# Performance work log

Measured on AMD Instinct MI355X. Metric: run time of the kernel, lower is better.

The kernel has to match this reference:

```python
import jax, jax.numpy as jnp
import numpy as np

N_NODES = 50000
N_EDGES = 1000000
D = 66
NEG_SLOPE = 0.2
EPS_BN = 1e-5


def _glorot(key, shape):
    fan = sum(shape)
    lim = jnp.sqrt(6.0 / fan)
    return jax.random.uniform(key, shape, jnp.float32, -lim, lim)


def setup_inputs() -> dict:
    key = jax.random.key(0)
    ks = jax.random.split(key, 40)
    inp = {
        'h': jax.random.normal(ks[0], (N_NODES, D), jnp.float32),
        'edge_index': jax.random.randint(ks[1], (2, N_EDGES), 0, N_NODES, jnp.int32),
        'edge_weight': jax.random.uniform(ks[2], (N_EDGES, 1), jnp.float32),
        'bn_gamma': jnp.ones((D,), jnp.float32),
        'bn_beta': jnp.zeros((D,), jnp.float32),
    }
    i = 3
    for l in (1, 2, 3):
        inp[f'W{l}'] = _glorot(ks[i], (D, D)); i += 1
        inp[f'b{l}'] = jnp.zeros((D,), jnp.float32)
        inp[f'att_src{l}'] = _glorot(ks[i], (D,)); i += 1
        inp[f'att_dst{l}'] = _glorot(ks[i], (D,)); i += 1
        inp[f'We{l}'] = _glorot(ks[i], (1, D)); i += 1
        inp[f'att_e{l}'] = _glorot(ks[i], (D,)); i += 1
    dims = [(D, D), (D, D), (D, D), (D, D), (D, 22)]
    for l, (din, dout) in enumerate(dims, start=1):
        inp[f'fc{l}_w'] = _glorot(ks[i], (din, dout)); i += 1
        inp[f'fc{l}_b'] = jnp.zeros((dout,), jnp.float32)
    return inp


def _gat_conv(h, src, dst, edge_weight, W, b, att_src, att_dst, We, att_e):
    x = h @ W                                     # [N, D]
    a_src = x @ att_src                           # [N]
    a_dst = x @ att_dst                           # [N]
    a_e = (edge_weight @ We) @ att_e              # [E]
    alpha = a_src[src] + a_dst[dst] + a_e         # [E]
    alpha = jnp.where(alpha > 0, alpha, NEG_SLOPE * alpha)
    # scatter-softmax over destination nodes
    m = jax.ops.segment_max(alpha, dst, num_segments=N_NODES)
    m = jnp.where(jnp.isfinite(m), m, 0.0)
    ex = jnp.exp(alpha - m[dst])
    denom = jax.ops.segment_sum(ex, dst, num_segments=N_NODES)
    coef = ex / (denom[dst] + 1e-16)              # [E]
    out = jax.ops.segment_sum(coef[:, None] * x[src], dst, num_segments=N_NODES)
    return out + b


def reference(h, edge_index, edge_weight, bn_gamma, bn_beta,
              W1, b1, att_src1, att_dst1, We1, att_e1,
              W2, b2, att_src2, att_dst2, We2, att_e2,
              W3, b3, att_src3, att_dst3, We3, att_e3,
              fc1_w, fc1_b, fc2_w, fc2_b, fc3_w, fc3_b,
              fc4_w, fc4_b, fc5_w, fc5_b):
    src, dst = edge_index[0], edge_index[1]
    # BatchNorm1d (training-mode batch statistics, biased variance)
    mean = h.mean(0)
    var = ((h - mean) ** 2).mean(0)
    x = (h - mean) * jax.lax.rsqrt(var + EPS_BN) * bn_gamma + bn_beta
    x = jax.nn.relu(_gat_conv(x, src, dst, edge_weight, W1, b1, att_src1, att_dst1, We1, att_e1))
    x = jax.nn.relu(_gat_conv(x, src, dst, edge_weight, W2, b2, att_src2, att_dst2, We2, att_e2))
    x = jax.nn.relu(_gat_conv(x, src, dst, edge_weight, W3, b3, att_src3, att_dst3, We3, att_e3))
    x = jax.nn.relu(x @ fc1_w + fc1_b)
    x = jax.nn.relu(x @ fc2_w + fc2_b)
    x = jax.nn.relu(x @ fc3_w + fc3_b)
    x = jax.nn.relu(x @ fc4_w + fc4_b)
    return x @ fc5_w + fc5_b
```

## Files before the change

kernel.cpp:

```cpp
#include <hip/hip_runtime.h>
#include <math.h>

#define D 66
#define SP 68
#define NEG_SLOPE 0.2f
#define CAP 6144

typedef short s8v __attribute__((ext_vector_type(8)));
typedef float f4v __attribute__((ext_vector_type(4)));

__device__ __forceinline__ float lrelu(float a){ return a > 0.f ? a : NEG_SLOPE * a; }
__device__ __forceinline__ void fma4(float4& a, float s, const float4& w){
  a.x = fmaf(s, w.x, a.x); a.y = fmaf(s, w.y, a.y);
  a.z = fmaf(s, w.z, a.z); a.w = fmaf(s, w.w, a.w);
}
__device__ __forceinline__ unsigned short bf16r(float f){
  unsigned u = __float_as_uint(f);
  u += 0x7FFFu + ((u >> 16) & 1u);
  return (unsigned short)(u >> 16);
}
__device__ __forceinline__ float bf16f(unsigned short b){
  return __uint_as_float(((unsigned)b) << 16);
}
__device__ __forceinline__ void split8(const float* p, s8v& a0, s8v& a1, s8v& a2){
  #pragma unroll
  for (int j = 0; j < 8; j++){
    float v = p[j];
    unsigned short b0 = bf16r(v);  float f0 = bf16f(b0);
    float r1 = v - f0;
    unsigned short b1 = bf16r(r1); float f1 = bf16f(b1);
    unsigned short b2 = bf16r(r1 - f1);
    a0[j] = (short)b0; a1[j] = (short)b1; a2[j] = (short)b2;
  }
}
#define MM6(acc, a0, a1, a2, b0v, b1v, b2v)                                \
  acc = __builtin_amdgcn_mfma_f32_16x16x32_bf16(a0, b0v, acc, 0, 0, 0);    \
  acc = __builtin_amdgcn_mfma_f32_16x16x32_bf16(a1, b0v, acc, 0, 0, 0);    \
  acc = __builtin_amdgcn_mfma_f32_16x16x32_bf16(a0, b1v, acc, 0, 0, 0);    \
  acc = __builtin_amdgcn_mfma_f32_16x16x32_bf16(a2, b0v, acc, 0, 0, 0);    \
  acc = __builtin_amdgcn_mfma_f32_16x16x32_bf16(a1, b1v, acc, 0, 0, 0);    \
  acc = __builtin_amdgcn_mfma_f32_16x16x32_bf16(a0, b2v, acc, 0, 0, 0);

__global__ __launch_bounds__(256) void k_bn_stats(const float* __restrict__ h,
                                                  float* __restrict__ sums, int n){
  __shared__ float ls[2 * D];
  int t = threadIdx.x;
  if (t < 2 * D) ls[t] = 0.f;
  __syncthreads();
  int rpb = (n + gridDim.x - 1) / gridDim.x;
  int r0 = blockIdx.x * rpb;
  int r1 = min(n, r0 + rpb);
  if (t < 3 * D){
    int c = t % D, seg = t / D;
    float s1 = 0.f, s2 = 0.f;
    for (int r = r0 + seg; r < r1; r += 3){
      float v = h[(size_t)r * D + c];
      s1 += v; s2 += v * v;
    }
    atomicAdd(&ls[c], s1);
    atomicAdd(&ls[D + c], s2);
  }
  __syncthreads();
  if (t < 2 * D) atomicAdd(&sums[t], ls[t]);
}

__global__ void k_bn_finalize(const float* __restrict__ sums,
                              const float* __restrict__ gamma, const float* __restrict__ beta,
                              const float* __restrict__ We1, const float* __restrict__ ae1,
                              const float* __restrict__ We2, const float* __restrict__ ae2,
                              const float* __restrict__ We3, const float* __restrict__ ae3,
                              float* __restrict__ misc, int n){
  int t = threadIdx.x;
  if (t < D){
    float mean = sums[t] / (float)n;
    float var  = sums[D + t] / (float)n - mean * mean;
    float inv  = rsqrtf(var + 1e-5f);
    float sc = gamma[t] * inv;
    misc[t] = sc;
    misc[D + t] = beta[t] - mean * sc;
  } else if (t == D){
    float c = 0.f; for (int d = 0; d < D; d++) c += We1[d] * ae1[d]; misc[2*D + 0] = c;
  } else if (t == D + 1){
    float c = 0.f; for (int d = 0; d < D; d++) c += We2[d] * ae2[d]; misc[2*D + 1] = c;
  } else if (t == D + 2){
    float c = 0.f; for (int d = 0; d < D; d++) c += We3[d] * ae3[d]; misc[2*D + 2] = c;
  }
}

__global__ __launch_bounds__(256) void k_bn_apply(const float* __restrict__ h, const float* __restrict__ misc,
                                                  float* __restrict__ x, int n){
  int i = blockIdx.x * 256 + threadIdx.x;
  int r = i / (SP/2), c2 = i - r * (SP/2);
  if (r >= n) return;
  int c = 2 * c2;
  float2 v = make_float2(0.f, 0.f);
  if (c < D){
    float2 hv = *(const float2*)&h[(size_t)r * D + c];
    v.x = hv.x * misc[c]     + misc[D + c];
    v.y = hv.y * misc[c + 1] + misc[D + c + 1];
  }
  *(float2*)&x[(size_t)r * SP + c] = v;
}

__global__ __launch_bounds__(256) void k_pack(const float* __restrict__ w0, const float* __restrict__ w1,
                                              const float* __restrict__ w2,
                                              short* __restrict__ W0, short* __restrict__ W1,
                                              short* __restrict__ W2){
  int tid = blockIdx.x * 256 + threadIdx.x;
  if (tid >= 3 * 15 * 64) return;
  int L = tid & 63;
  int ct = (tid >> 6) % 15;
  int lay = tid / 960;
  const float* w = (lay == 0) ? w0 : ((lay == 1) ? w1 : w2);
  int c = ct / 5, t = ct % 5;
  int nn = t * 16 + (L & 15);
  int kb = c * 32 + (L >> 4) * 8;
  #pragma unroll
  for (int j = 0; j < 8; j++){
    int k = kb + j;
    float v = (k < D && nn < D) ? w[k * D + nn] : 0.f;
    unsigned short b0 = bf16r(v);  float f0 = bf16f(b0);
    float r1 = v - f0;
    unsigned short b1 = bf16r(r1); float f1 = bf16f(b1);
    unsigned short b2 = bf16r(r1 - f1);
    W0[tid * 8 + j] = (short)b0;
    W1[tid * 8 + j] = (short)b1;
    W2[tid * 8 + j] = (short)b2;
  }
}

__global__ __launch_bounds__(256) void k_packfc(const float* __restrict__ w0, const float* __restrict__ w1,
                                                const float* __restrict__ w2, const float* __restrict__ w3,
                                                const float* __restrict__ w4,
                                                short* __restrict__ W0, short* __restrict__ W1,
                                                short* __restrict__ W2){
  int tid = blockIdx.x * 256 + threadIdx.x;
  if (tid >= 5 * 15 * 64) return;
  int L = tid & 63;
  int ct = (tid >> 6) % 15;
  int lay = tid / 960;
  const float* w = (lay == 0) ? w0 : (lay == 1) ? w1 : (lay == 2) ? w2 : (lay == 3) ? w3 : w4;
  int ncol = (lay == 4) ? 22 : D;
  int c = ct / 5, t = ct % 5;
  int nn = t * 16 + (L & 15);
  int kb = c * 32 + (L >> 4) * 8;
  #pragma unroll
  for (int j = 0; j < 8; j++){
    int k = kb + j;
    float v = (k < D && nn < ncol) ? w[k * ncol + nn] : 0.f;
    unsigned short b0 = bf16r(v);  float f0 = bf16f(b0);
    float r1 = v - f0;
    unsigned short b1 = bf16r(r1); float f1 = bf16f(b1);
    unsigned short b2 = bf16r(r1 - f1);
    W0[tid * 8 + j] = (short)b0;
    W1[tid * 8 + j] = (short)b1;
    W2[tid * 8 + j] = (short)b2;
  }
}

__global__ __launch_bounds__(256) void k_hist(const int* __restrict__ dst,
                                              int* __restrict__ bhist, int E){
  __shared__ int h[256];
  int t = threadIdx.x;
  h[t] = 0;
  __syncthreads();
  int stride = gridDim.x * blockDim.x;
  for (int e = blockIdx.x * blockDim.x + t; e < E; e += stride)
    atomicAdd(&h[dst[e] >> 8], 1);
  __syncthreads();
  if (h[t]) atomicAdd(&bhist[t], h[t]);
}

__global__ void k_bscan(const int* __restrict__ bhist, int* __restrict__ bbase,
                        int* __restrict__ gcur, int* __restrict__ rowptr, int N, int E){
  __shared__ int sh[256];
  int t = threadIdx.x;
  int v = bhist[t];
  sh[t] = v; __syncthreads();
  for (int o = 1; o < 256; o <<= 1){
    int u = (t >= o) ? sh[t - o] : 0;
    __syncthreads();
    sh[t] += u;
    __syncthreads();
  }
  int ex = sh[t] - v;
  bbase[t] = ex;
  gcur[t] = ex;
  if (t == 255){ bbase[256] = sh[255]; rowptr[N] = E; }
}

#define PCHUNK 4096
__global__ __launch_bounds__(256) void k_part(const int* __restrict__ src, const int* __restrict__ dst,
                                              const float* __restrict__ ew,
                                              int* __restrict__ gcur, int2* __restrict__ tmp, int E){
  __shared__ int hist[256];
  __shared__ int base[256];
  int t = threadIdx.x;
  int e0 = blockIdx.x * PCHUNK;
  int eend = min(E, e0 + PCHUNK);
  hist[t] = 0;
  __syncthreads();
  for (int e = e0 + t; e < eend; e += 256)
    atomicAdd(&hist[dst[e] >> 8], 1);
  __syncthreads();
  if (hist[t] > 0) base[t] = atomicAdd(&gcur[t], hist[t]);
  hist[t] = 0;
  __syncthreads();
  for (int e = e0 + t; e < eend; e += 256){
    int d = dst[e];
    int b = d >> 8;
    int off = atomicAdd(&hist[b], 1);
    tmp[base[b] + off] = make_int2((src[e] & 0xffff) | ((d & 255) << 16), __float_as_int(ew[e]));
  }
}

__global__ __launch_bounds__(256) void k_bsort(const int2* __restrict__ tmp, const int* __restrict__ bbase,
                                               int2* __restrict__ epair, int* __restrict__ rowptr, int N){
  __shared__ int2 ebuf[CAP];
  __shared__ int lcnt[256];
  __shared__ int sc[256];
  __shared__ int lcur[256];
  int b = blockIdx.x, t = threadIdx.x;
  int s0 = bbase[b], s1 = bbase[b + 1];
  int cnt = s1 - s0;
  lcnt[t] = 0;
  __syncthreads();
  for (int j = t; j < cnt; j += 256){
    int2 e = tmp[s0 + j];
    if (j < CAP) ebuf[j] = e;
    atomicAdd(&lcnt[(e.x >> 16) & 255], 1);
  }
  __syncthreads();
  int v = lcnt[t];
  sc[t] = v; __syncthreads();
  for (int o = 1; o < 256; o <<= 1){
    int u = (t >= o) ? sc[t - o] : 0;
    __syncthreads();
    sc[t] += u;
    __syncthreads();
  }
  int ex = sc[t] - v;
  int node = (b << 8) + t;
  if (node < N) rowptr[node] = s0 + ex;
  lcur[t] = ex;
  __syncthreads();
  for (int j = t; j < cnt; j += 256){
    int2 e = (j < CAP) ? ebuf[j] : tmp[s0 + j];
    int i = (e.x >> 16) & 255;
    int p = atomicAdd(&lcur[i], 1);
    epair[s0 + p] = make_int2(e.x & 0xffff, e.y);
  }
}

__global__ __launch_bounds__(256) void k_mm(const float* __restrict__ X,
    const short* __restrict__ W0, const short* __restrict__ W1, const short* __restrict__ W2,
    const float* __restrict__ att_s, const float* __restrict__ att_d,
    float* __restrict__ Y, float* __restrict__ a_src, float* __restrict__ a_dst, int n){
  const int wv = threadIdx.x >> 6, L = threadIdx.x & 63;
  const int quad = L >> 4, m = L & 15;
  const int row0 = blockIdx.x * 64 + wv * 16;
  const int lrow = min(row0 + m, n - 1);
  const float* xr = X + (size_t)lrow * SP;
  f4v acc[5];
  #pragma unroll
  for (int t = 0; t < 5; t++) acc[t] = (f4v){0.f,0.f,0.f,0.f};

  #pragma unroll
  for (int c = 0; c < 3; c++){
    float xv[8];
    if (c < 2){
      float4 p0 = *(const float4*)&xr[c * 32 + quad * 8];
      float4 p1 = *(const float4*)&xr[c * 32 + quad * 8 + 4];
      xv[0] = p0.x; xv[1] = p0.y; xv[2] = p0.z; xv[3] = p0.w;
      xv[4] = p1.x; xv[5] = p1.y; xv[6] = p1.z; xv[7] = p1.w;
    } else {
      float4 p0 = make_float4(0.f, 0.f, 0.f, 0.f);
      if (quad == 0) p0 = *(const float4*)&xr[64];
      xv[0] = p0.x; xv[1] = p0.y; xv[2] = p0.z; xv[3] = p0.w;
      xv[4] = 0.f; xv[5] = 0.f; xv[6] = 0.f; xv[7] = 0.f;
    }
    s8v a0, a1, a2;
    split8(xv, a0, a1, a2);
    const short* b0p = W0 + (c * 5) * 512 + L * 8;
    const short* b1p = W1 + (c * 5) * 512 + L * 8;
    const short* b2p = W2 + (c * 5) * 512 + L * 8;
    #pragma unroll
    for (int t = 0; t < 5; t++){
      s8v b0v = *(const s8v*)(b0p + t * 512);
      s8v b1v = *(const s8v*)(b1p + t * 512);
      s8v b2v = *(const s8v*)(b2p + t * 512);
      MM6(acc[t], a0, a1, a2, b0v, b1v, b2v)
    }
  }

  float ps[4] = {0.f,0.f,0.f,0.f}, pd[4] = {0.f,0.f,0.f,0.f};
  #pragma unroll
  for (int t = 0; t < 5; t++){
    int col = t * 16 + m;
    float as_v = 0.f, ad_v = 0.f;
    if (col < D){ as_v = att_s[col]; ad_v = att_d[col]; }
    #pragma unroll
    for (int r = 0; r < 4; r++){
      ps[r] += acc[t][r] * as_v;
      pd[r] += acc[t][r] * ad_v;
    }
  }
  #pragma unroll
  for (int r = 0; r < 4; r++){
    int rw = row0 + quad * 4 + r;
    if (rw < n){
      float* yr = Y + (size_t)rw * SP;
      #pragma unroll
      for (int t = 0; t < 4; t++) yr[t * 16 + m] = acc[t][r];
      if (m < 4) yr[64 + m] = (m < 2) ? acc[4][r] : 0.f;
    }
  }
  #pragma unroll
  for (int o = 1; o <= 8; o <<= 1){
    #pragma unroll
    for (int r = 0; r < 4; r++){
      ps[r] += __shfl_xor(ps[r], o);
      pd[r] += __shfl_xor(pd[r], o);
    }
  }
  if (m == 0){
    #pragma unroll
    for (int r = 0; r < 4; r++){
      int rw = row0 + quad * 4 + r;
      if (rw < n){ a_src[rw] = ps[r]; a_dst[rw] = pd[r]; }
    }
  }
}

template<bool LAST>
__global__ __launch_bounds__(256) void k_fcl(const float* __restrict__ X,
    const short* __restrict__ W0, const short* __restrict__ W1, const short* __restrict__ W2,
    const float* __restrict__ bias,
    float* __restrict__ Y, int n){
  const int wv = threadIdx.x >> 6, L = threadIdx.x & 63;
  const int quad = L >> 4, m = L & 15;
  const int row0 = blockIdx.x * 64 + wv * 16;
  const int lrow = min(row0 + m, n - 1);
  const float* xr = X + (size_t)lrow * SP;
  constexpr int NT = LAST ? 2 : 5;
  f4v acc[NT];
  #pragma unroll
  for (int t = 0; t < NT; t++) acc[t] = (f4v){0.f,0.f,0.f,0.f};

  #pragma unroll
  for (int c = 0; c < 3; c++){
    float xv[8];
    if (c < 2){
      float4 p0 = *(const float4*)&xr[c * 32 + quad * 8];
      float4 p1 = *(const float4*)&xr[c * 32 + quad * 8 + 4];
      xv[0] = p0.x; xv[1] = p0.y; xv[2] = p0.z; xv[3] = p0.w;
      xv[4] = p1.x; xv[5] = p1.y; xv[6] = p1.z; xv[7] = p1.w;
    } else {
      float4 p0 = make_float4(0.f, 0.f, 0.f, 0.f);
      if (quad == 0) p0 = *(const float4*)&xr[64];
      xv[0] = p0.x; xv[1] = p0.y; xv[2] = p0.z; xv[3] = p0.w;
      xv[4] = 0.f; xv[5] = 0.f; xv[6] = 0.f; xv[7] = 0.f;
    }
    s8v a0, a1, a2;
    split8(xv, a0, a1, a2);
    const short* b0p = W0 + (c * 5) * 512 + L * 8;
    const short* b1p = W1 + (c * 5) * 512 + L * 8;
    const short* b2p = W2 + (c * 5) * 512 + L * 8;
    #pragma unroll
    for (int t = 0; t < NT; t++){
      s8v b0v = *(const s8v*)(b0p + t * 512);
      s8v b1v = *(const s8v*)(b1p + t * 512);
      s8v b2v = *(const s8v*)(b2p + t * 512);
      MM6(acc[t], a0, a1, a2, b0v, b1v, b2v)
    }
  }

  if (!LAST){
    #pragma unroll
    for (int r = 0; r < 4; r++){
      int rw = row0 + quad * 4 + r;
      if (rw < n){
        float* yr = Y + (size_t)rw * SP;
        #pragma unroll
        for (int t = 0; t < 4; t++){
          int col = t * 16 + m;
          float v = acc[t][r] + bias[col];
          yr[col] = v > 0.f ? v : 0.f;
        }
        if (m < 4){
          float v = 0.f;
          if (m < 2){
            v = acc[4][r] + bias[64 + m];
            v = v > 0.f ? v : 0.f;
          }
          yr[64 + m] = v;
        }
      }
    }
  } else {
    #pragma unroll
    for (int t = 0; t < 2; t++){
      int col = t * 16 + m;
      #pragma unroll
      for (int r = 0; r < 4; r++){
        int rw = row0 + quad * 4 + r;
        if (col < 22 && rw < n) Y[(size_t)rw * 22 + col] = acc[t][r] + bias[col];
      }
    }
  }
}

__global__ __launch_bounds__(256) void k_agg(const float* __restrict__ y,
                                             const float* __restrict__ a_src, const float* __restrict__ a_dst,
                                             const int* __restrict__ rowptr, const int2* __restrict__ epair,
                                             const float* __restrict__ misc, int cidx,
                                             const float* __restrict__ bias,
                                             float* __restrict__ xout, int n){
  const int wid  = (int)((blockIdx.x * (size_t)blockDim.x + threadIdx.x) >> 6);
  const int lane = threadIdx.x & 63;
  if (wid >= n) return;
  const int beg = rowptr[wid];
  const int deg = rowptr[wid + 1] - beg;
  const float ce  = misc[2 * D + cidx];
  const float adn = a_dst[wid];
  const int g = lane >> 4, q = lane & 15;

  float4 vacc = make_float4(0.f, 0.f, 0.f, 0.f);
  float2 tacc = make_float2(0.f, 0.f);

  if (deg <= 64){
    int s = 0; float al = -INFINITY;
    bool act = lane < deg;
    if (act){
      int2 ep = epair[beg + lane];
      s = ep.x;
      al = lrelu(a_src[s] + adn + ce * __int_as_float(ep.y));
    }
    float m = al;
    #pragma unroll
    for (int o = 32; o; o >>= 1) m = fmaxf(m, __shfl_xor(m, o));
    float ex = act ? __expf(al - m) : 0.f;
    float sum = ex;
    #pragma unroll
    for (int o = 32; o; o >>= 1) sum += __shfl_xor(sum, o);
    float coef = ex * (1.f / (sum + 1e-16f));
    for (int e0 = 0; e0 < deg; e0 += 4){
      int e = e0 + g;
      int   st = __shfl(s, e);
      float ct = __shfl(coef, e);
      const float* row = y + (size_t)st * SP;
      float4 yv = *(const float4*)&row[4 * q];
      fma4(vacc, ct, yv);
      if (q == 0){
        float2 tv = *(const float2*)&row[64];
        tacc.x += ct * tv.x; tacc.y += ct * tv.y;
      }
    }
  } else {
    float m = -INFINITY;
    for (int j0 = 0; j0 < deg; j0 += 64){
      int j = j0 + lane;
      if (j < deg){
        int2 ep = epair[beg + j];
        m = fmaxf(m, lrelu(a_src[ep.x] + adn + ce * __int_as_float(ep.y)));
      }
    }
    #pragma unroll
    for (int o = 32; o; o >>= 1) m = fmaxf(m, __shfl_xor(m, o));
    float sum = 0.f;
    for (int j0 = 0; j0 < deg; j0 += 64){
      int j = j0 + lane;
      if (j < deg){
        int2 ep = epair[beg + j];
        sum += __expf(lrelu(a_src[ep.x] + adn + ce * __int_as_float(ep.y)) - m);
      }
    }
    #pragma unroll
    for (int o = 32; o; o >>= 1) sum += __shfl_xor(sum, o);
    float inv = 1.f / (sum + 1e-16f);
    for (int j0 = 0; j0 < deg; j0 += 64){
      int cnt = min(64, deg - j0);
      int s = 0; float coef = 0.f;
      if (lane < cnt){
        int2 ep = epair[beg + j0 + lane];
        s = ep.x;
        coef = __expf(lrelu(a_src[s] + adn + ce * __int_as_float(ep.y)) - m) * inv;
      }
      for (int e0 = 0; e0 < cnt; e0 += 4){
        int e = e0 + g;
        int   st = __shfl(s, e);
        float ct = __shfl(coef, e);
        const float* row = y + (size_t)st * SP;
        float4 yv = *(const float4*)&row[4 * q];
        fma4(vacc, ct, yv);
        if (q == 0){
          float2 tv = *(const float2*)&row[64];
          tacc.x += ct * tv.x; tacc.y += ct * tv.y;
        }
      }
    }
  }

  #pragma unroll
  for (int o = 16; o <= 32; o <<= 1){
    vacc.x += __shfl_xor(vacc.x, o);
    vacc.y += __shfl_xor(vacc.y, o);
    vacc.z += __shfl_xor(vacc.z, o);
    vacc.w += __shfl_xor(vacc.w, o);
    tacc.x += __shfl_xor(tacc.x, o);
    tacc.y += __shfl_xor(tacc.y, o);
  }
  float* orow = xout + (size_t)wid * SP;
  if (lane < 16){
    float4 v;
    v.x = vacc.x + bias[4*lane+0]; v.x = v.x > 0.f ? v.x : 0.f;
    v.y = vacc.y + bias[4*lane+1]; v.y = v.y > 0.f ? v.y : 0.f;
    v.z = vacc.z + bias[4*lane+2]; v.z = v.z > 0.f ? v.z : 0.f;
    v.w = vacc.w + bias[4*lane+3]; v.w = v.w > 0.f ? v.w : 0.f;
    *(float4*)&orow[4 * lane] = v;
  }
  if (lane == 0){
    float4 tv;
    tv.x = tacc.x + bias[64]; tv.x = tv.x > 0.f ? tv.x : 0.f;
    tv.y = tacc.y + bias[65]; tv.y = tv.y > 0.f ? tv.y : 0.f;
    tv.z = 0.f; tv.w = 0.f;
    *(float4*)&orow[64] = tv;
  }
}

extern "C" void kernel_launch(void* const* d_in, const int* in_sizes, int n_in,
                              void* d_out, int out_size, void* d_ws, size_t ws_size,
                              hipStream_t stream){
  const float* h     = (const float*)d_in[0];
  const int*   ei    = (const int*)  d_in[1];
  const float* ew    = (const float*)d_in[2];
  const float* gamma = (const float*)d_in[3];
  const float* beta  = (const float*)d_in[4];
  const float *Wl[3], *bl[3], *asl[3], *adl[3], *Wel[3], *ael[3];
  int idx = 5;
  for (int l = 0; l < 3; l++){
    Wl[l]  = (const float*)d_in[idx++];
    bl[l]  = (const float*)d_in[idx++];
    asl[l] = (const float*)d_in[idx++];
    adl[l] = (const float*)d_in[idx++];
    Wel[l] = (const float*)d_in[idx++];
    ael[l] = (const float*)d_in[idx++];
  }
  const float *fw[5], *fb[5];
  for (int l = 0; l < 5; l++){ fw[l] = (const float*)d_in[idx++]; fb[l] = (const float*)d_in[idx++]; }

  int N = in_sizes[0] / D;
  int E = in_sizes[1] / 2;
  const int* src  = ei;
  const int* dstp = ei + E;

  char* base = (char*)d_ws;
  size_t o = 0;
  auto alloc = [&](size_t b){ size_t r = o; o += (b + 255) & ~(size_t)255; return r; };
  float*  bufA   = (float*)(base + alloc((size_t)N * SP * 4));
  float*  bufB   = (float*)(base + alloc((size_t)N * SP * 4));
  float*  a_src  = (float*)(base + alloc((size_t)N * 4));
  float*  a_dst  = (float*)(base + alloc((size_t)N * 4));
  float*  misc   = (float*)(base + alloc(512 * 4));
  float*  sums   = (float*)(base + alloc(2 * D * 4));
  int*    rowptr = (int*)  (base + alloc((size_t)(N + 1) * 4));
  int*    bhist  = (int*)  (base + alloc(256 * 4));
  int*    bbase  = (int*)  (base + alloc(257 * 4));
  int*    gcur   = (int*)  (base + alloc(256 * 4));
  int2*   epair  = (int2*) (base + alloc((size_t)E * 8));
  short*  W0p    = (short*)(base + alloc(3 * 7680 * 2));
  short*  W1p    = (short*)(base + alloc(3 * 7680 * 2));
  short*  W2p    = (short*)(base + alloc(3 * 7680 * 2));
  short*  FW0p   = (short*)(base + alloc(5 * 7680 * 2));
  short*  FW1p   = (short*)(base + alloc(5 * 7680 * 2));
  short*  FW2p   = (short*)(base + alloc(5 * 7680 * 2));
  int2*   tmp    = (int2*)bufB;

  hipMemsetAsync(sums, 0, 2 * D * 4, stream);
  hipMemsetAsync(bhist, 0, 256 * 4, stream);

  k_bn_stats<<<256, 256, 0, stream>>>(h, sums, N);
  k_bn_finalize<<<1, 128, 0, stream>>>(sums, gamma, beta, Wel[0], ael[0], Wel[1], ael[1], Wel[2], ael[2], misc, N);
  k_pack<<<12, 256, 0, stream>>>(Wl[0], Wl[1], Wl[2], W0p, W1p, W2p);
  k_packfc<<<19, 256, 0, stream>>>(fw[0], fw[1], fw[2], fw[3], fw[4], FW0p, FW1p, FW2p);

  int NB = (N + 255) >> 8;
  k_hist<<<256, 256, 0, stream>>>(dstp, bhist, E);
  k_bscan<<<1, 256, 0, stream>>>(bhist, bbase, gcur, rowptr, N, E);
  k_part<<<(E + PCHUNK - 1) / PCHUNK, 256, 0, stream>>>(src, dstp, ew, gcur, tmp, E);
  k_bsort<<<NB, 256, 0, stream>>>(tmp, bbase, epair, rowptr, N);

  int bnb = ((size_t)N * (SP/2) + 255) / 256;
  k_bn_apply<<<bnb, 256, 0, stream>>>(h, misc, bufA, N);

  int gb = (N + 63) / 64;
  int ab = (N + 3) / 4;

  for (int l = 0; l < 3; l++){
    k_mm<<<gb, 256, 0, stream>>>(bufA, W0p + l * 7680, W1p + l * 7680, W2p + l * 7680,
                                 asl[l], adl[l], bufB, a_src, a_dst, N);
    k_agg<<<ab, 256, 0, stream>>>(bufB, a_src, a_dst, rowptr, epair, misc, l, bl[l], bufA, N);
  }

  k_fcl<false><<<gb, 256, 0, stream>>>(bufA, FW0p + 0 * 7680, FW1p + 0 * 7680, FW2p + 0 * 7680, fb[0], bufB, N);
  k_fcl<false><<<gb, 256, 0, stream>>>(bufB, FW0p + 1 * 7680, FW1p + 1 * 7680, FW2p + 1 * 7680, fb[1], bufA, N);
  k_fcl<false><<<gb, 256, 0, stream>>>(bufA, FW0p + 2 * 7680, FW1p + 2 * 7680, FW2p + 2 * 7680, fb[2], bufB, N);
  k_fcl<false><<<gb, 256, 0, stream>>>(bufB, FW0p + 3 * 7680, FW1p + 3 * 7680, FW2p + 3 * 7680, fb[3], bufA, N);
  k_fcl<true ><<<gb, 256, 0, stream>>>(bufA, FW0p + 4 * 7680, FW1p + 4 * 7680, FW2p + 4 * 7680, fb[4], (float*)d_out, N);
}
```

Measured before the change: 490.3 us.

## Fuse five FC layers into one kernel and widen aggregation edge groups

The five separate fully-connected layer launches are replaced by one kernel that keeps each 64-row tile's intermediate activations in shared memory across layers. This removes four launches and the global-memory round trips of the intermediates. The FC biases are packed into a padded buffer by the weight-pack kernel. Separately, the GAT aggregation now processes 8 edges per step with 8 lanes per row, each lane loading two float4s, instead of 4 edges with 16 lanes. This aims to give more gathers in flight per wave, at the cost of more register use and an extra shuffle-reduction stage.

```diff
diff --git a/kernel.cpp b/kernel.cpp
--- a/kernel.cpp
+++ b/kernel.cpp
@@ -132,29 +132,39 @@
 __global__ __launch_bounds__(256) void k_packfc(const float* __restrict__ w0, const float* __restrict__ w1,
                                                 const float* __restrict__ w2, const float* __restrict__ w3,
                                                 const float* __restrict__ w4,
+                                                const float* __restrict__ b0, const float* __restrict__ b1,
+                                                const float* __restrict__ b2, const float* __restrict__ b3,
+                                                const float* __restrict__ b4,
                                                 short* __restrict__ W0, short* __restrict__ W1,
-                                                short* __restrict__ W2){
+                                                short* __restrict__ W2, float* __restrict__ bpack){
   int tid = blockIdx.x * 256 + threadIdx.x;
-  if (tid >= 5 * 15 * 64) return;
-  int L = tid & 63;
-  int ct = (tid >> 6) % 15;
-  int lay = tid / 960;
-  const float* w = (lay == 0) ? w0 : (lay == 1) ? w1 : (lay == 2) ? w2 : (lay == 3) ? w3 : w4;
-  int ncol = (lay == 4) ? 22 : D;
-  int c = ct / 5, t = ct % 5;
-  int nn = t * 16 + (L & 15);
-  int kb = c * 32 + (L >> 4) * 8;
-  #pragma unroll
-  for (int j = 0; j < 8; j++){
-    int k = kb + j;
-    float v = (k < D && nn < ncol) ? w[k * ncol + nn] : 0.f;
-    unsigned short b0 = bf16r(v);  float f0 = bf16f(b0);
-    float r1 = v - f0;
-    unsigned short b1 = bf16r(r1); float f1 = bf16f(b1);
-    unsigned short b2 = bf16r(r1 - f1);
-    W0[tid * 8 + j] = (short)b0;
-    W1[tid * 8 + j] = (short)b1;
-    W2[tid * 8 + j] = (short)b2;
+  if (tid < 5 * 15 * 64){
+    int L = tid & 63;
+    int ct = (tid >> 6) % 15;
+    int lay = tid / 960;
+    const float* w = (lay == 0) ? w0 : (lay == 1) ? w1 : (lay == 2) ? w2 : (lay == 3) ? w3 : w4;
+    int ncol = (lay == 4) ? 22 : D;
+    int c = ct / 5, t = ct % 5;
+    int nn = t * 16 + (L & 15);
+    int kb = c * 32 + (L >> 4) * 8;
+    #pragma unroll
+    for (int j = 0; j < 8; j++){
+      int k = kb + j;
+      float v = (k < D && nn < ncol) ? w[k * ncol + nn] : 0.f;
+      unsigned short bb0 = bf16r(v);  float f0 = bf16f(bb0);
+      float r1 = v - f0;
+      unsigned short bb1 = bf16r(r1); float f1 = bf16f(bb1);
+      unsigned short bb2 = bf16r(r1 - f1);
+      W0[tid * 8 + j] = (short)bb0;
+      W1[tid * 8 + j] = (short)bb1;
+      W2[tid * 8 + j] = (short)bb2;
+    }
+  } else if (tid < 5 * 15 * 64 + 400){
+    int i = tid - 5 * 15 * 64;
+    int lay = i / 80, col = i % 80;
+    const float* b = (lay == 0) ? b0 : (lay == 1) ? b1 : (lay == 2) ? b2 : (lay == 3) ? b3 : b4;
+    int ncol = (lay == 4) ? 22 : D;
+    bpack[i] = (col < ncol) ? b[col] : 0.f;
   }
 }
 
@@ -332,79 +342,82 @@
   }
 }
 
-template<bool LAST>
-__global__ __launch_bounds__(256) void k_fcl(const float* __restrict__ X,
+#define FST 84
+__global__ __launch_bounds__(256) void k_fcmm(const float* __restrict__ X,
     const short* __restrict__ W0, const short* __restrict__ W1, const short* __restrict__ W2,
-    const float* __restrict__ bias,
-    float* __restrict__ Y, int n){
+    const float* __restrict__ bpack, float* __restrict__ out, int n){
+  __shared__ __align__(16) float xs[4][16][FST];
   const int wv = threadIdx.x >> 6, L = threadIdx.x & 63;
   const int quad = L >> 4, m = L & 15;
   const int row0 = blockIdx.x * 64 + wv * 16;
   const int lrow = min(row0 + m, n - 1);
   const float* xr = X + (size_t)lrow * SP;
-  constexpr int NT = LAST ? 2 : 5;
-  f4v acc[NT];
-  #pragma unroll
-  for (int t = 0; t < NT; t++) acc[t] = (f4v){0.f,0.f,0.f,0.f};
-
-  #pragma unroll
-  for (int c = 0; c < 3; c++){
-    float xv[8];
-    if (c < 2){
-      float4 p0 = *(const float4*)&xr[c * 32 + quad * 8];
-      float4 p1 = *(const float4*)&xr[c * 32 + quad * 8 + 4];
-      xv[0] = p0.x; xv[1] = p0.y; xv[2] = p0.z; xv[3] = p0.w;
-      xv[4] = p1.x; xv[5] = p1.y; xv[6] = p1.z; xv[7] = p1.w;
+
+  for (int l = 0; l < 5; l++){
+    const int NTl = (l == 4) ? 2 : 5;
+    f4v acc[5];
+    #pragma unroll
+    for (int t = 0; t < 5; t++) acc[t] = (f4v){0.f,0.f,0.f,0.f};
+    #pragma unroll
+    for (int c = 0; c < 3; c++){
+      float xv[8];
+      if (l == 0){
+        if (c < 2){
+          float4 p0 = *(const float4*)&xr[c * 32 + quad * 8];
+          float4 p1 = *(const float4*)&xr[c * 32 + quad * 8 + 4];
+          xv[0] = p0.x; xv[1] = p0.y; xv[2] = p0.z; xv[3] = p0.w;
+          xv[4] = p1.x; xv[5] = p1.y; xv[6] = p1.z; xv[7] = p1.w;
+        } else {
+          float4 p0 = make_float4(0.f, 0.f, 0.f, 0.f);
+          if (quad == 0) p0 = *(const float4*)&xr[64];
+          xv[0] = p0.x; xv[1] = p0.y; xv[2] = p0.z; xv[3] = p0.w;
+          xv[4] = 0.f; xv[5] = 0.f; xv[6] = 0.f; xv[7] = 0.f;
+        }
+      } else {
+        if (c == 2 && quad >= 2){
+          #pragma unroll
+          for (int j = 0; j < 8; j++) xv[j] = 0.f;
+        } else {
+          float4 p0 = *(const float4*)&xs[wv][m][c * 32 + quad * 8];
+          float4 p1 = *(const float4*)&xs[wv][m][c * 32 + quad * 8 + 4];
+          xv[0] = p0.x; xv[1] = p0.y; xv[2] = p0.z; xv[3] = p0.w;
+          xv[4] = p1.x; xv[5] = p1.y; xv[6] = p1.z; xv[7] = p1.w;
+        }
+      }
+      s8v a0, a1, a2;
+      split8(xv, a0, a1, a2);
+      const short* b0p = W0 + ((l * 3 + c) * 5) * 512 + L * 8;
+      const short* b1p = W1 + ((l * 3 + c) * 5) * 512 + L * 8;
+      const short* b2p = W2 + ((l * 3 + c) * 5) * 512 + L * 8;
+      for (int t = 0; t < NTl; t++){
+        s8v b0v = *(const s8v*)(b0p + t * 512);
+        s8v b1v = *(const s8v*)(b1p + t * 512);
+        s8v b2v = *(const s8v*)(b2p + t * 512);
+        MM6(acc[t], a0, a1, a2, b0v, b1v, b2v)
+      }
+    }
+    if (l < 4){
+      __syncthreads();
+      #pragma unroll
+      for (int t = 0; t < 5; t++){
+        int col = t * 16 + m;
+        float bv = bpack[l * 80 + col];
+        #pragma unroll
+        for (int r = 0; r < 4; r++){
+          float v = acc[t][r] + bv;
+          xs[wv][quad * 4 + r][col] = v > 0.f ? v : 0.f;
+        }
+      }
+      __syncthreads();
     } else {
-      float4 p0 = make_float4(0.f, 0.f, 0.f, 0.f);
-      if (quad == 0) p0 = *(const float4*)&xr[64];
-      xv[0] = p0.x; xv[1] = p0.y; xv[2] = p0.z; xv[3] = p0.w;
-      xv[4] = 0.f; xv[5] = 0.f; xv[6] = 0.f; xv[7] = 0.f;
-    }
-    s8v a0, a1, a2;
-    split8(xv, a0, a1, a2);
-    const short* b0p = W0 + (c * 5) * 512 + L * 8;
-    const short* b1p = W1 + (c * 5) * 512 + L * 8;
-    const short* b2p = W2 + (c * 5) * 512 + L * 8;
-    #pragma unroll
-    for (int t = 0; t < NT; t++){
-      s8v b0v = *(const s8v*)(b0p + t * 512);
-      s8v b1v = *(const s8v*)(b1p + t * 512);
-      s8v b2v = *(const s8v*)(b2p + t * 512);
-      MM6(acc[t], a0, a1, a2, b0v, b1v, b2v)
-    }
-  }
-
-  if (!LAST){
-    #pragma unroll
-    for (int r = 0; r < 4; r++){
-      int rw = row0 + quad * 4 + r;
-      if (rw < n){
-        float* yr = Y + (size_t)rw * SP;
+      #pragma unroll
+      for (int t = 0; t < 2; t++){
+        int col = t * 16 + m;
         #pragma unroll
-        for (int t = 0; t < 4; t++){
-          int col = t * 16 + m;
-          float v = acc[t][r] + bias[col];
-          yr[col] = v > 0.f ? v : 0.f;
+        for (int r = 0; r < 4; r++){
+          int rw = row0 + quad * 4 + r;
+          if (col < 22 && rw < n) out[(size_t)rw * 22 + col] = acc[t][r] + bpack[4 * 80 + col];
         }
-        if (m < 4){
-          float v = 0.f;
-          if (m < 2){
-            v = acc[4][r] + bias[64 + m];
-            v = v > 0.f ? v : 0.f;
-          }
-          yr[64 + m] = v;
-        }
-      }
-    }
-  } else {
-    #pragma unroll
-    for (int t = 0; t < 2; t++){
-      int col = t * 16 + m;
-      #pragma unroll
-      for (int r = 0; r < 4; r++){
-        int rw = row0 + quad * 4 + r;
-        if (col < 22 && rw < n) Y[(size_t)rw * 22 + col] = acc[t][r] + bias[col];
       }
     }
   }
@@ -423,10 +436,11 @@
   const int deg = rowptr[wid + 1] - beg;
   const float ce  = misc[2 * D + cidx];
   const float adn = a_dst[wid];
-  const int g = lane >> 4, q = lane & 15;
-
-  float4 vacc = make_float4(0.f, 0.f, 0.f, 0.f);
-  float2 tacc = make_float2(0.f, 0.f);
+  const int g = lane >> 3, q = lane & 7;
+
+  float4 accA = make_float4(0.f,0.f,0.f,0.f);
+  float4 accB = make_float4(0.f,0.f,0.f,0.f);
+  float2 tacc = make_float2(0.f,0.f);
 
   if (deg <= 64){
     int s = 0; float al = -INFINITY;
@@ -436,43 +450,47 @@
       s = ep.x;
       al = lrelu(a_src[s] + adn + ce * __int_as_float(ep.y));
     }
-    float m = al;
-    #pragma unroll
-    for (int o = 32; o; o >>= 1) m = fmaxf(m, __shfl_xor(m, o));
-    float ex = act ? __expf(al - m) : 0.f;
+    float mx = al;
+    #pragma unroll
+    for (int o = 32; o; o >>= 1) mx = fmaxf(mx, __shfl_xor(mx, o));
+    float ex = act ? __expf(al - mx) : 0.f;
     float sum = ex;
     #pragma unroll
     for (int o = 32; o; o >>= 1) sum += __shfl_xor(sum, o);
     float coef = ex * (1.f / (sum + 1e-16f));
-    for (int e0 = 0; e0 < deg; e0 += 4){
+    for (int e0 = 0; e0 < deg; e0 += 8){
       int e = e0 + g;
       int   st = __shfl(s, e);
       float ct = __shfl(coef, e);
-      const float* row = y + (size_t)st * SP;
-      float4 yv = *(const float4*)&row[4 * q];
-      fma4(vacc, ct, yv);
-      if (q == 0){
-        float2 tv = *(const float2*)&row[64];
-        tacc.x += ct * tv.x; tacc.y += ct * tv.y;
+      if (e < deg){
+        const float* row = y + (size_t)st * SP;
+        float4 y0 = *(const float4*)&row[4 * q];
+        float4 y1 = *(const float4*)&row[32 + 4 * q];
+        fma4(accA, ct, y0);
+        fma4(accB, ct, y1);
+        if (q == 0){
+          float2 tv = *(const float2*)&row[64];
+          tacc.x += ct * tv.x; tacc.y += ct * tv.y;
+        }
       }
     }
   } else {
-    float m = -INFINITY;
+    float mx = -INFINITY;
     for (int j0 = 0; j0 < deg; j0 += 64){
       int j = j0 + lane;
       if (j < deg){
         int2 ep = epair[beg + j];
-        m = fmaxf(m, lrelu(a_src[ep.x] + adn + ce * __int_as_float(ep.y)));
-      }
-    }
-    #pragma unroll
-    for (int o = 32; o; o >>= 1) m = fmaxf(m, __shfl_xor(m, o));
+        mx = fmaxf(mx, lrelu(a_src[ep.x] + adn + ce * __int_as_float(ep.y)));
+      }
+    }
+    #pragma unroll
+    for (int o = 32; o; o >>= 1) mx = fmaxf(mx, __shfl_xor(mx, o));
     float sum = 0.f;
     for (int j0 = 0; j0 < deg; j0 += 64){
       int j = j0 + lane;
       if (j < deg){
         int2 ep = epair[beg + j];
-        sum += __expf(lrelu(a_src[ep.x] + adn + ce * __int_as_float(ep.y)) - m);
+        sum += __expf(lrelu(a_src[ep.x] + adn + ce * __int_as_float(ep.y)) - mx);
       }
     }
     #pragma unroll
@@ -480,44 +498,56 @@
     float inv = 1.f / (sum + 1e-16f);
     for (int j0 = 0; j0 < deg; j0 += 64){
       int cnt = min(64, deg - j0);
-      int s = 0; float coef = 0.f;
+      int s = 0; float ex = 0.f;
       if (lane < cnt){
         int2 ep = epair[beg + j0 + lane];
         s = ep.x;
-        coef = __expf(lrelu(a_src[s] + adn + ce * __int_as_float(ep.y)) - m) * inv;
-      }
-      for (int e0 = 0; e0 < cnt; e0 += 4){
+        ex = __expf(lrelu(a_src[s] + adn + ce * __int_as_float(ep.y)) - mx);
+      }
+      float coef = ex * inv;
+      for (int e0 = 0; e0 < cnt; e0 += 8){
         int e = e0 + g;
         int   st = __shfl(s, e);
         float ct = __shfl(coef, e);
-        const float* row = y + (size_t)st * SP;
-        float4 yv = *(const float4*)&row[4 * q];
-        fma4(vacc, ct, yv);
-        if (q == 0){
-          float2 tv = *(const float2*)&row[64];
-          tacc.x += ct * tv.x; tacc.y += ct * tv.y;
+        if (e < cnt){
+          const float* row = y + (size_t)st * SP;
+          float4 y0 = *(const float4*)&row[4 * q];
+          float4 y1 = *(const float4*)&row[32 + 4 * q];
+          fma4(accA, ct, y0);
+          fma4(accB, ct, y1);
+          if (q == 0){
+            float2 tv = *(const float2*)&row[64];
+            tacc.x += ct * tv.x; tacc.y += ct * tv.y;
+          }
         }
       }
     }
   }
 
   #pragma unroll
-  for (int o = 16; o <= 32; o <<= 1){
-    vacc.x += __shfl_xor(vacc.x, o);
-    vacc.y += __shfl_xor(vacc.y, o);
-    vacc.z += __shfl_xor(vacc.z, o);
-    vacc.w += __shfl_xor(vacc.w, o);
-    tacc.x += __shfl_xor(tacc.x, o);
-    tacc.y += __shfl_xor(tacc.y, o);
+  for (int o = 8; o <= 32; o <<= 1){
+    accA.x += __shfl_xor(accA.x, o); accA.y += __shfl_xor(accA.y, o);
+    accA.z += __shfl_xor(accA.z, o); accA.w += __shfl_xor(accA.w, o);
+    accB.x += __shfl_xor(accB.x, o); accB.y += __shfl_xor(accB.y, o);
+    accB.z += __shfl_xor(accB.z, o); accB.w += __shfl_xor(accB.w, o);
+    tacc.x += __shfl_xor(tacc.x, o); tacc.y += __shfl_xor(tacc.y, o);
   }
   float* orow = xout + (size_t)wid * SP;
-  if (lane < 16){
+  if (lane < 8){
     float4 v;
-    v.x = vacc.x + bias[4*lane+0]; v.x = v.x > 0.f ? v.x : 0.f;
-    v.y = vacc.y + bias[4*lane+1]; v.y = v.y > 0.f ? v.y : 0.f;
-    v.z = vacc.z + bias[4*lane+2]; v.z = v.z > 0.f ? v.z : 0.f;
-    v.w = vacc.w + bias[4*lane+3]; v.w = v.w > 0.f ? v.w : 0.f;
+    v.x = accA.x + bias[4*lane+0]; v.x = v.x > 0.f ? v.x : 0.f;
+    v.y = accA.y + bias[4*lane+1]; v.y = v.y > 0.f ? v.y : 0.f;
+    v.z = accA.z + bias[4*lane+2]; v.z = v.z > 0.f ? v.z : 0.f;
+    v.w = accA.w + bias[4*lane+3]; v.w = v.w > 0.f ? v.w : 0.f;
     *(float4*)&orow[4 * lane] = v;
+  } else if (lane < 16){
+    int qq = lane - 8;
+    float4 v;
+    v.x = accB.x + bias[32+4*qq+0]; v.x = v.x > 0.f ? v.x : 0.f;
+    v.y = accB.y + bias[32+4*qq+1]; v.y = v.y > 0.f ? v.y : 0.f;
+    v.z = accB.z + bias[32+4*qq+2]; v.z = v.z > 0.f ? v.z : 0.f;
+    v.w = accB.w + bias[32+4*qq+3]; v.w = v.w > 0.f ? v.w : 0.f;
+    *(float4*)&orow[32 + 4 * qq] = v;
   }
   if (lane == 0){
     float4 tv;
@@ -574,6 +604,7 @@
   short*  FW0p   = (short*)(base + alloc(5 * 7680 * 2));
   short*  FW1p   = (short*)(base + alloc(5 * 7680 * 2));
   short*  FW2p   = (short*)(base + alloc(5 * 7680 * 2));
+  float*  bpack  = (float*)(base + alloc(400 * 4));
   int2*   tmp    = (int2*)bufB;
 
   hipMemsetAsync(sums, 0, 2 * D * 4, stream);
@@ -582,7 +613,9 @@
   k_bn_stats<<<256, 256, 0, stream>>>(h, sums, N);
   k_bn_finalize<<<1, 128, 0, stream>>>(sums, gamma, beta, Wel[0], ael[0], Wel[1], ael[1], Wel[2], ael[2], misc, N);
   k_pack<<<12, 256, 0, stream>>>(Wl[0], Wl[1], Wl[2], W0p, W1p, W2p);
-  k_packfc<<<19, 256, 0, stream>>>(fw[0], fw[1], fw[2], fw[3], fw[4], FW0p, FW1p, FW2p);
+  k_packfc<<<21, 256, 0, stream>>>(fw[0], fw[1], fw[2], fw[3], fw[4],
+                                   fb[0], fb[1], fb[2], fb[3], fb[4],
+                                   FW0p, FW1p, FW2p, bpack);
 
   int NB = (N + 255) >> 8;
   k_hist<<<256, 256, 0, stream>>>(dstp, bhist, E);
@@ -602,9 +635,5 @@
     k_agg<<<ab, 256, 0, stream>>>(bufB, a_src, a_dst, rowptr, epair, misc, l, bl[l], bufA, N);
   }
 
-  k_fcl<false><<<gb, 256, 0, stream>>>(bufA, FW0p + 0 * 7680, FW1p + 0 * 7680, FW2p + 0 * 7680, fb[0], bufB, N);
-  k_fcl<false><<<gb, 256, 0, stream>>>(bufB, FW0p + 1 * 7680, FW1p + 1 * 7680, FW2p + 1 * 7680, fb[1], bufA, N);
-  k_fcl<false><<<gb, 256, 0, stream>>>(bufA, FW0p + 2 * 7680, FW1p + 2 * 7680, FW2p + 2 * 7680, fb[2], bufB, N);
-  k_fcl<false><<<gb, 256, 0, stream>>>(bufB, FW0p + 3 * 7680, FW1p + 3 * 7680, FW2p + 3 * 7680, fb[3], bufA, N);
-  k_fcl<true ><<<gb, 256, 0, stream>>>(bufA, FW0p + 4 * 7680, FW1p + 4 * 7680, FW2p + 4 * 7680, fb[4], (float*)d_out, N);
-}
+  k_fcmm<<<gb, 256, 0, stream>>>(bufA, FW0p, FW1p, FW2p, bpack, (float*)d_out, N);
+}
```

Measured after the change: 475.4 us. 3.0% less time.
